# Kernel optimization log

Hardware: AMD Instinct MI355X
Metric: run time of the kernel (lower is better)

## Reference

```python
import jax, jax.numpy as jnp
import numpy as np

KLD_SCALE = 10.0
COMMITMENT_COST = 0.1


def setup_inputs() -> dict:
    key = jax.random.key(0)
    k1, k2 = jax.random.split(key)
    z = jax.random.normal(k1, (32, 2048, 64), dtype=jnp.float32)
    codebook = jax.random.normal(k2, (1024, 64), dtype=jnp.float32)
    return {"z": z, "codebook": codebook}


def reference(z, codebook):
    B, N, D = z.shape
    z_e = z.reshape(B * N, D)                          # (M, D)
    # squared euclidean distance: ||z||^2 - 2 z.E^T + ||E||^2
    dist = (
        jnp.sum(z_e * z_e, axis=1, keepdims=True)
        - 2.0 * (z_e @ codebook.T)
        + jnp.sum(codebook * codebook, axis=1)[None, :]
    )                                                  # (M, K)
    ind = jnp.argmin(dist, axis=1)                     # (M,)
    z_q = codebook[ind]                                # (M, D) gather
    latent_loss = (
        COMMITMENT_COST * jnp.mean((jax.lax.stop_gradient(z_q) - z_e) ** 2)
        + jnp.mean((z_q - jax.lax.stop_gradient(z_e)) ** 2)
    ) * KLD_SCALE
    # straight-through estimator
    z_q_st = z_e + jax.lax.stop_gradient(z_q - z_e)
    return z_q_st.reshape(B, N, D), latent_loss
```

## Files before the change

### kernel.cpp

```cpp
#include <hip/hip_runtime.h>
#include <hip/hip_bf16.h>
#include <float.h>

#define DIMS 64
#define KC 1024
#define M_TOTAL 65536
#define TAU 4e-3f

typedef __attribute__((ext_vector_type(8))) short bf16x8;
typedef __attribute__((ext_vector_type(4))) float f32x4;

#define SE_OFF   0
#define CTL_OFF  1024
#define PART_OFF 2048
#define PBH_OFF  4096
#define PBL_OFF  36864
#define WL_OFF   69632
#define IDX_OFF  135168

__device__ inline short f2bf(float x) {
  union { __hip_bfloat16 h; short s; } u;
  u.h = __float2bfloat16(x);
  return u.s;
}
__device__ inline float bf2f(short x) {
  union { short s; __hip_bfloat16 h; } u;
  u.s = x;
  return __bfloat162float(u.h);
}

__device__ inline void gload_lds16(const void* g, void* l) {
  __builtin_amdgcn_global_load_lds(
      (const __attribute__((address_space(1))) void*)g,
      (__attribute__((address_space(3))) void*)l, 16, 0, 0);
}

__global__ __launch_bounds__(256) void k_prep(const float* __restrict__ cb,
                                              float* __restrict__ se,
                                              unsigned int* __restrict__ ctl,
                                              unsigned short* __restrict__ pbh,
                                              unsigned short* __restrict__ pbl) {
  const int tid = blockIdx.x * 256 + threadIdx.x;
  if (tid < 4) ctl[tid] = 0;
  const int l = tid & 63;
  const int s = (tid >> 6) & 1;
  const int tt = tid >> 7;
  const int code = tt * 16 + (l & 15);
  const int k = s * 32 + (l >> 4) * 8;
  const float* p = cb + (size_t)code * DIMS + k;
  float v[8];
  ((float4*)v)[0] = ((const float4*)p)[0];
  ((float4*)v)[1] = ((const float4*)p)[1];
  bf16x8 h, lo;
#pragma unroll
  for (int j = 0; j < 8; ++j) {
    short hj = f2bf(v[j]);
    h[j] = hj;
    lo[j] = f2bf(v[j] - bf2f(hj));
  }
  *(bf16x8*)(pbh + (size_t)tid * 8) = h;
  *(bf16x8*)(pbl + (size_t)tid * 8) = lo;

  if (tid < KC) {
    const float4* q = (const float4*)(cb + (size_t)tid * DIMS);
    float a0 = 0.f, a1 = 0.f, a2 = 0.f, a3 = 0.f;
#pragma unroll
    for (int i = 0; i < DIMS / 4; ++i) {
      float4 u = q[i];
      a0 = fmaf(u.x, u.x, a0);
      a1 = fmaf(u.y, u.y, a1);
      a2 = fmaf(u.z, u.z, a2);
      a3 = fmaf(u.w, u.w, a3);
    }
    se[tid] = (a0 + a1) + (a2 + a3);
  }
}

__global__ __launch_bounds__(256, 2) void k_dist(const float* __restrict__ z,
                                                 const unsigned short* __restrict__ pbh,
                                                 const unsigned short* __restrict__ pbl,
                                                 const float* __restrict__ se,
                                                 int* __restrict__ idxo,
                                                 int* __restrict__ wl,
                                                 unsigned int* __restrict__ ctl) {
  __shared__ bf16x8 sB[2][2][256];
  const int l = threadIdx.x & 63;
  const int w = threadIdx.x >> 6;
  const int r0 = blockIdx.x * 128 + w * 32;
  const int col = l & 15;
  const int g = l >> 4;

  bf16x8 ah[2][2], al[2][2];
#pragma unroll
  for (int rs = 0; rs < 2; ++rs) {
    const float* zp = z + (size_t)(r0 + rs * 16 + col) * DIMS + g * 8;
#pragma unroll
    for (int ks = 0; ks < 2; ++ks) {
      float v[8];
      ((float4*)v)[0] = ((const float4*)(zp + ks * 32))[0];
      ((float4*)v)[1] = ((const float4*)(zp + ks * 32))[1];
#pragma unroll
      for (int j = 0; j < 8; ++j) {
        short hj = f2bf(v[j]);
        ah[rs][ks][j] = hj;
        al[rs][ks][j] = f2bf(v[j] - bf2f(hj));
      }
    }
  }

  float m1[2][4], m2[2][4];
  int bt[2][4];
#pragma unroll
  for (int rs = 0; rs < 2; ++rs)
#pragma unroll
    for (int j = 0; j < 4; ++j) {
      m1[rs][j] = FLT_MAX;
      m2[rs][j] = FLT_MAX;
      bt[rs][j] = 0;
    }

  {
    const int f = w * 64 + l;
    gload_lds16(pbh + (size_t)f * 8, &sB[0][0][w * 64]);
    gload_lds16(pbl + (size_t)f * 8, &sB[0][1][w * 64]);
  }
  __syncthreads();

  int cur = 0;
  for (int c = 0; c < 32; ++c) {
    if (c + 1 < 32) {
      const size_t f = (size_t)(c + 1) * 256 + w * 64 + l;
      gload_lds16(pbh + f * 8, &sB[cur ^ 1][0][w * 64]);
      gload_lds16(pbl + f * 8, &sB[cur ^ 1][1][w * 64]);
    }
#pragma unroll
    for (int tt = 0; tt < 2; ++tt) {
      const int t = c * 2 + tt;
      bf16x8 bh0 = sB[cur][0][tt * 128 + l];
      bf16x8 bh1 = sB[cur][0][tt * 128 + 64 + l];
      bf16x8 bl0 = sB[cur][1][tt * 128 + l];
      bf16x8 bl1 = sB[cur][1][tt * 128 + 64 + l];
      const float sec = se[t * 16 + col];
      f32x4 acc0 = {0.f, 0.f, 0.f, 0.f};
      f32x4 acc1 = {0.f, 0.f, 0.f, 0.f};
      acc0 = __builtin_amdgcn_mfma_f32_16x16x32_bf16(ah[0][0], bh0, acc0, 0, 0, 0);
      acc1 = __builtin_amdgcn_mfma_f32_16x16x32_bf16(ah[1][0], bh0, acc1, 0, 0, 0);
      acc0 = __builtin_amdgcn_mfma_f32_16x16x32_bf16(ah[0][1], bh1, acc0, 0, 0, 0);
      acc1 = __builtin_amdgcn_mfma_f32_16x16x32_bf16(ah[1][1], bh1, acc1, 0, 0, 0);
      acc0 = __builtin_amdgcn_mfma_f32_16x16x32_bf16(ah[0][0], bl0, acc0, 0, 0, 0);
      acc1 = __builtin_amdgcn_mfma_f32_16x16x32_bf16(ah[1][0], bl0, acc1, 0, 0, 0);
      acc0 = __builtin_amdgcn_mfma_f32_16x16x32_bf16(ah[0][1], bl1, acc0, 0, 0, 0);
      acc1 = __builtin_amdgcn_mfma_f32_16x16x32_bf16(ah[1][1], bl1, acc1, 0, 0, 0);
      acc0 = __builtin_amdgcn_mfma_f32_16x16x32_bf16(al[0][0], bh0, acc0, 0, 0, 0);
      acc1 = __builtin_amdgcn_mfma_f32_16x16x32_bf16(al[1][0], bh0, acc1, 0, 0, 0);
      acc0 = __builtin_amdgcn_mfma_f32_16x16x32_bf16(al[0][1], bh1, acc0, 0, 0, 0);
      acc1 = __builtin_amdgcn_mfma_f32_16x16x32_bf16(al[1][1], bh1, acc1, 0, 0, 0);
#pragma unroll
      for (int rs = 0; rs < 2; ++rs) {
        const f32x4 acc = rs ? acc1 : acc0;
#pragma unroll
        for (int j = 0; j < 4; ++j) {
          float d = fmaf(-2.f, acc[j], sec);
          float nm2 = __builtin_amdgcn_fmed3f(d, m1[rs][j], m2[rs][j]);
          bool lt = d < m1[rs][j];
          m1[rs][j] = lt ? d : m1[rs][j];
          bt[rs][j] = lt ? t : bt[rs][j];
          m2[rs][j] = nm2;
        }
      }
    }
    __syncthreads();
    cur ^= 1;
  }

#pragma unroll
  for (int rs = 0; rs < 2; ++rs)
#pragma unroll
    for (int j = 0; j < 4; ++j) {
      float m1j = m1[rs][j], m2j = m2[rs][j];
      int ij = bt[rs][j] * 16 + col;
      for (int msk = 1; msk <= 8; msk <<= 1) {
        float o1 = __shfl_xor(m1j, msk);
        float o2 = __shfl_xor(m2j, msk);
        int oi = __shfl_xor(ij, msk);
        bool take = (o1 < m1j) || (o1 == m1j && oi < ij);
        float hi = take ? m1j : o1;
        m2j = fminf(fminf(m2j, o2), hi);
        m1j = take ? o1 : m1j;
        ij = take ? oi : ij;
      }
      if (col == 0) {
        const int row = r0 + rs * 16 + g * 4 + j;
        idxo[row] = ij;
        if (m2j - m1j < TAU) {
          int p = atomicAdd((int*)ctl, 1);
          wl[p] = row;
        }
      }
    }
}

__global__ __launch_bounds__(256) void k_refine(const float* __restrict__ z,
                                                const float* __restrict__ cb,
                                                const int* __restrict__ wl,
                                                const unsigned int* __restrict__ ctl,
                                                int* __restrict__ idxo) {
  __shared__ float zz[64];
  __shared__ double sd[256];
  __shared__ int si[256];
  const int t = threadIdx.x;
  const int n = (int)ctl[0];
  for (int wi = blockIdx.x; wi < n; wi += 1024) {
    const int row = wl[wi];
    if (t < 16) ((float4*)zz)[t] = ((const float4*)(z + (size_t)row * DIMS))[t];
    __syncthreads();
    const int c0 = t * 4;
    double accd[4] = {0.0, 0.0, 0.0, 0.0};
    for (int ch = 0; ch < 4; ++ch) {
      float zr[16];
#pragma unroll
      for (int q = 0; q < 4; ++q) ((float4*)zr)[q] = ((float4*)zz)[ch * 4 + q];
#pragma unroll
      for (int cc = 0; cc < 4; ++cc) {
        const float* e = cb + (size_t)(c0 + cc) * DIMS + ch * 16;
#pragma unroll
        for (int q = 0; q < 16; ++q) {
          double df = (double)zr[q] - (double)e[q];
          accd[cc] = fma(df, df, accd[cc]);
        }
      }
    }
    double best = 1e300;
    int bi = 0;
#pragma unroll
    for (int cc = 0; cc < 4; ++cc)
      if (accd[cc] < best) { best = accd[cc]; bi = c0 + cc; }
    sd[t] = best;
    si[t] = bi;
    __syncthreads();
    for (int off = 128; off > 0; off >>= 1) {
      if (t < off) {
        double ob = sd[t + off];
        int oi = si[t + off];
        if (ob < sd[t] || (ob == sd[t] && oi < si[t])) { sd[t] = ob; si[t] = oi; }
      }
      __syncthreads();
    }
    if (t == 0) idxo[row] = si[0];
    __syncthreads();
  }
}

__global__ __launch_bounds__(256) void k_out(const float* __restrict__ z,
                                             const float* __restrict__ cb,
                                             const int* __restrict__ idxi,
                                             float* __restrict__ out,
                                             float* __restrict__ partials) {
  const int tid = blockIdx.x * 256 + threadIdx.x;
  const int row = tid >> 2;
  const int q = tid & 3;
  const int code = idxi[row];
  const float4* zp = (const float4*)(z + (size_t)row * DIMS + q * 16);
  const float4* ep = (const float4*)(cb + (size_t)code * DIMS + q * 16);
  float4* op = (float4*)(out + (size_t)row * DIMS + q * 16);
  float sse = 0.f;
#pragma unroll
  for (int i = 0; i < 4; ++i) {
    float4 v = zp[i], e = ep[i];
    float dx = e.x - v.x, dy = e.y - v.y, dz = e.z - v.z, dw = e.w - v.w;
    sse = fmaf(dx, dx, sse);
    sse = fmaf(dy, dy, sse);
    sse = fmaf(dz, dz, sse);
    sse = fmaf(dw, dw, sse);
    float4 o;
    o.x = v.x + dx;
    o.y = v.y + dy;
    o.z = v.z + dz;
    o.w = v.w + dw;
    op[i] = o;
  }
  __shared__ float sh[256];
  sh[threadIdx.x] = sse;
  __syncthreads();
  for (int off = 128; off > 0; off >>= 1) {
    if (threadIdx.x < off) sh[threadIdx.x] += sh[threadIdx.x + off];
    __syncthreads();
  }
  if (threadIdx.x == 0) partials[blockIdx.x] = sh[0];
}

__global__ __launch_bounds__(256) void k_loss(const float* __restrict__ partials,
                                              float* __restrict__ out) {
  __shared__ float sh[256];
  const int t = threadIdx.x;
  sh[t] = partials[t] + partials[t + 256] + partials[t + 512] + partials[t + 768];
  __syncthreads();
  for (int off = 128; off > 0; off >>= 1) {
    if (t < off) sh[t] += sh[t + off];
    __syncthreads();
  }
  if (t == 0) {
    out[(size_t)M_TOTAL * DIMS] = sh[0] * (11.0f / (float)((size_t)M_TOTAL * DIMS));
  }
}

extern "C" void kernel_launch(void* const* d_in, const int* in_sizes, int n_in,
                              void* d_out, int out_size, void* d_ws, size_t ws_size,
                              hipStream_t stream) {
  const float* z = (const float*)d_in[0];
  const float* cb = (const float*)d_in[1];
  float* out = (float*)d_out;
  float* ws = (float*)d_ws;

  float* se = ws + SE_OFF;
  unsigned int* ctl = (unsigned int*)(ws + CTL_OFF);
  float* partials = ws + PART_OFF;
  unsigned short* pbh = (unsigned short*)(ws + PBH_OFF);
  unsigned short* pbl = (unsigned short*)(ws + PBL_OFF);
  int* wl = (int*)(ws + WL_OFF);
  int* idx = (int*)(ws + IDX_OFF);

  k_prep<<<32, 256, 0, stream>>>(cb, se, ctl, pbh, pbl);
  k_dist<<<M_TOTAL / 128, 256, 0, stream>>>(z, pbh, pbl, se, idx, wl, ctl);
  k_refine<<<1024, 256, 0, stream>>>(z, cb, wl, ctl, idx);
  k_out<<<M_TOTAL / 64, 256, 0, stream>>>(z, cb, idx, out, partials);
  k_loss<<<1, 256, 0, stream>>>(partials, out);
}
```

Before: 60.03 us.

## Split codebook scan across two blocks per row tile and merge top-2 results

The distance kernel now runs twice as many blocks, each scanning half of the codebook for the same 128-row tile. Each block writes its partial best and second-best distances and index to workspace, and a new merge kernel combines the halves and builds the near-tie refine worklist. The launch bound is raised to 4 waves per SIMD to allow more blocks resident. The aim is more parallelism and occupancy on a grid of 512 blocks. The cost is an extra kernel launch, extra global traffic for the partial results, and the z fragments being loaded and converted twice. The worklist now reuses the bf16 codebook buffer region, which is safe only because that buffer is no longer read after k_dist.

```diff
diff --git a/kernel.cpp b/kernel.cpp
--- a/kernel.cpp
+++ b/kernel.cpp
@@ -15,8 +15,9 @@
 #define PART_OFF 2048
 #define PBH_OFF  4096
 #define PBL_OFF  36864
-#define WL_OFF   69632
-#define IDX_OFF  135168
+#define M1_OFF   69632
+#define M2_OFF   200704
+#define IDX_OFF  331776
 
 __device__ inline short f2bf(float x) {
   union { __hip_bfloat16 h; short s; } u;
@@ -76,17 +77,19 @@
   }
 }
 
-__global__ __launch_bounds__(256, 2) void k_dist(const float* __restrict__ z,
+__global__ __launch_bounds__(256, 4) void k_dist(const float* __restrict__ z,
                                                  const unsigned short* __restrict__ pbh,
                                                  const unsigned short* __restrict__ pbl,
                                                  const float* __restrict__ se,
-                                                 int* __restrict__ idxo,
-                                                 int* __restrict__ wl,
-                                                 unsigned int* __restrict__ ctl) {
+                                                 float* __restrict__ m1o,
+                                                 float* __restrict__ m2o,
+                                                 int* __restrict__ idxo) {
   __shared__ bf16x8 sB[2][2][256];
   const int l = threadIdx.x & 63;
   const int w = threadIdx.x >> 6;
-  const int r0 = blockIdx.x * 128 + w * 32;
+  const int split = blockIdx.x & 1;
+  const int rb = blockIdx.x >> 1;
+  const int r0 = rb * 128 + w * 32;
   const int col = l & 15;
   const int g = l >> 4;
 
@@ -119,28 +122,29 @@
       bt[rs][j] = 0;
     }
 
+  const int cg0 = split * 16;
   {
-    const int f = w * 64 + l;
-    gload_lds16(pbh + (size_t)f * 8, &sB[0][0][w * 64]);
-    gload_lds16(pbl + (size_t)f * 8, &sB[0][1][w * 64]);
+    const size_t f = (size_t)cg0 * 256 + w * 64 + l;
+    gload_lds16(pbh + f * 8, &sB[0][0][w * 64]);
+    gload_lds16(pbl + f * 8, &sB[0][1][w * 64]);
   }
   __syncthreads();
 
   int cur = 0;
-  for (int c = 0; c < 32; ++c) {
-    if (c + 1 < 32) {
-      const size_t f = (size_t)(c + 1) * 256 + w * 64 + l;
+  for (int c = 0; c < 16; ++c) {
+    if (c + 1 < 16) {
+      const size_t f = (size_t)(cg0 + c + 1) * 256 + w * 64 + l;
       gload_lds16(pbh + f * 8, &sB[cur ^ 1][0][w * 64]);
       gload_lds16(pbl + f * 8, &sB[cur ^ 1][1][w * 64]);
     }
 #pragma unroll
     for (int tt = 0; tt < 2; ++tt) {
-      const int t = c * 2 + tt;
+      const int gt = cg0 * 2 + c * 2 + tt;
       bf16x8 bh0 = sB[cur][0][tt * 128 + l];
       bf16x8 bh1 = sB[cur][0][tt * 128 + 64 + l];
       bf16x8 bl0 = sB[cur][1][tt * 128 + l];
       bf16x8 bl1 = sB[cur][1][tt * 128 + 64 + l];
-      const float sec = se[t * 16 + col];
+      const float sec = se[gt * 16 + col];
       f32x4 acc0 = {0.f, 0.f, 0.f, 0.f};
       f32x4 acc1 = {0.f, 0.f, 0.f, 0.f};
       acc0 = __builtin_amdgcn_mfma_f32_16x16x32_bf16(ah[0][0], bh0, acc0, 0, 0, 0);
@@ -164,7 +168,7 @@
           float nm2 = __builtin_amdgcn_fmed3f(d, m1[rs][j], m2[rs][j]);
           bool lt = d < m1[rs][j];
           m1[rs][j] = lt ? d : m1[rs][j];
-          bt[rs][j] = lt ? t : bt[rs][j];
+          bt[rs][j] = lt ? gt : bt[rs][j];
           m2[rs][j] = nm2;
         }
       }
@@ -190,14 +194,30 @@
         ij = take ? oi : ij;
       }
       if (col == 0) {
-        const int row = r0 + rs * 16 + g * 4 + j;
-        idxo[row] = ij;
-        if (m2j - m1j < TAU) {
-          int p = atomicAdd((int*)ctl, 1);
-          wl[p] = row;
-        }
-      }
-    }
+        const int o = split * M_TOTAL + r0 + rs * 16 + g * 4 + j;
+        m1o[o] = m1j;
+        m2o[o] = m2j;
+        idxo[o] = ij;
+      }
+    }
+}
+
+__global__ __launch_bounds__(256) void k_merge(const float* __restrict__ m1s,
+                                               const float* __restrict__ m2s,
+                                               int* __restrict__ idxs,
+                                               int* __restrict__ wl,
+                                               unsigned int* __restrict__ ctl) {
+  const int row = blockIdx.x * 256 + threadIdx.x;
+  const float a1 = m1s[row], b1 = m1s[M_TOTAL + row];
+  const float a2 = m2s[row], b2 = m2s[M_TOTAL + row];
+  const int ia = idxs[row], ib = idxs[M_TOTAL + row];
+  const float m1 = fminf(a1, b1);
+  const float m2 = fminf(fmaxf(a1, b1), fminf(a2, b2));
+  idxs[row] = (b1 < a1) ? ib : ia;
+  if (m2 - m1 < TAU) {
+    int p = atomicAdd((int*)ctl, 1);
+    wl[p] = row;
+  }
 }
 
 __global__ __launch_bounds__(256) void k_refine(const float* __restrict__ z,
@@ -317,11 +337,14 @@
   float* partials = ws + PART_OFF;
   unsigned short* pbh = (unsigned short*)(ws + PBH_OFF);
   unsigned short* pbl = (unsigned short*)(ws + PBL_OFF);
-  int* wl = (int*)(ws + WL_OFF);
+  float* m1s = ws + M1_OFF;
+  float* m2s = ws + M2_OFF;
   int* idx = (int*)(ws + IDX_OFF);
+  int* wl = (int*)(ws + PBH_OFF);
 
   k_prep<<<32, 256, 0, stream>>>(cb, se, ctl, pbh, pbl);
-  k_dist<<<M_TOTAL / 128, 256, 0, stream>>>(z, pbh, pbl, se, idx, wl, ctl);
+  k_dist<<<(M_TOTAL / 128) * 2, 256, 0, stream>>>(z, pbh, pbl, se, m1s, m2s, idx);
+  k_merge<<<M_TOTAL / 256, 256, 0, stream>>>(m1s, m2s, idx, wl, ctl);
   k_refine<<<1024, 256, 0, stream>>>(z, cb, wl, ctl, idx);
   k_out<<<M_TOTAL / 64, 256, 0, stream>>>(z, cb, idx, out, partials);
   k_loss<<<1, 256, 0, stream>>>(partials, out);
```

Result: slower. 64.38 us (+7.3%).
